# Kernel optimization log

Measured on AMD Instinct MI355X. Metric: run time of the kernel, lower is better.

Reference implementation:

```python
import jax, jax.numpy as jnp
import numpy as np

PLANE_SIZE = 512
N_LEVELS = 8
FEATURE_DIM = 16
N_PTS = 524288


def setup_inputs() -> dict:
    key = jax.random.key(0)
    k1, k2, k3 = jax.random.split(key, 3)
    x = jax.random.uniform(k1, (N_PTS, 3), dtype=jnp.float32)
    # per-point float mip level bias in [0, n_levels-1]
    level = jax.random.uniform(k2, (N_PTS, 1), dtype=jnp.float32) * (N_LEVELS - 1)
    fm = jax.random.uniform(k3, (3, PLANE_SIZE, PLANE_SIZE, FEATURE_DIM),
                            minval=-0.01, maxval=0.01, dtype=jnp.float32)
    return {"x": x, "level": level, "fm": fm, "n_levels": N_LEVELS}


def _bilinear(flat_pyr, offsets, sizes, uv, lvl_i):
    # flat_pyr: (3, T, C) concatenated mip levels; uv: (3, N, 2); lvl_i: (3, N) int32
    size = sizes[lvl_i]                      # (3, N) texture size at this mip
    fsize = size.astype(uv.dtype)
    px = uv[..., 0] * fsize - 0.5            # u -> width axis (nvdiffrast convention)
    py = uv[..., 1] * fsize - 0.5            # v -> height axis
    x0 = jnp.floor(px)
    y0 = jnp.floor(py)
    fx = (px - x0)[..., None]
    fy = (py - y0)[..., None]
    x0i = x0.astype(jnp.int32)
    y0i = y0.astype(jnp.int32)
    xa = jnp.clip(x0i, 0, size - 1)          # boundary_mode='clamp'
    xb = jnp.clip(x0i + 1, 0, size - 1)
    ya = jnp.clip(y0i, 0, size - 1)
    yb = jnp.clip(y0i + 1, 0, size - 1)
    base = offsets[lvl_i]
    p = jnp.arange(3)[:, None]
    g = lambda yy, xx: flat_pyr[p, base + yy * size + xx]   # (3, N, C) gather
    f00 = g(ya, xa); f01 = g(ya, xb); f10 = g(yb, xa); f11 = g(yb, xb)
    return (f00 * (1 - fx) + f01 * fx) * (1 - fy) + (f10 * (1 - fx) + f11 * fx) * fy


def reference(x, level, fm, n_levels):
    N = x.shape[0]
    C = fm.shape[-1]
    # build mip pyramid via 2x2 box filter (nvdiffrast auto-mips)
    levels = [fm]
    for _ in range(n_levels - 1):
        t = levels[-1]
        s = t.shape[1]
        levels.append(t.reshape(3, s // 2, 2, s // 2, 2, C).mean(axis=(2, 4)))
    sizes_list = [l.shape[1] for l in levels]
    offsets = jnp.asarray(np.cumsum([0] + [s * s for s in sizes_list[:-1]]), jnp.int32)
    sizes = jnp.asarray(sizes_list, jnp.int32)
    flat_pyr = jnp.concatenate([l.reshape(3, -1, C) for l in levels], axis=1)  # (3, T, C)
    # tri-plane decomposition: plane0 sees (y,z), plane1 (x,z), plane2 (x,y)
    uv = jnp.stack([x[:, [1, 2]], x[:, [0, 2]], x[:, [0, 1]]], axis=0)  # (3, N, 2)
    max_mip = n_levels - 1
    lvl = jnp.clip(jnp.broadcast_to(level.reshape(1, N), (3, N)), 0.0, float(max_mip))
    l0 = jnp.floor(lvl)
    f = (lvl - l0)[..., None]                # (3, N, 1) level fraction
    l0i = l0.astype(jnp.int32)
    l1i = jnp.minimum(l0i + 1, max_mip)
    s0 = _bilinear(flat_pyr, offsets, sizes, uv, l0i)
    s1 = _bilinear(flat_pyr, offsets, sizes, uv, l1i)
    enc = s0 * (1 - f) + s1 * f              # (3, N, C) trilinear (mip-lerped)
    # permute(1,2,0,3).view(N, 3C): per point, concat plane0|plane1|plane2 features
    return jnp.transpose(enc, (1, 0, 2)).reshape(N, 3 * C)
```

## Files before the change

### kernel.cpp

```cpp
#include <hip/hip_runtime.h>


#define FM_PLANE_STRIDE (262144 * 16)
#define WS_PLANE_STRIDE (87376 * 16)

__device__ __forceinline__ float4 ld4(const float* p) {
    return *reinterpret_cast<const float4*>(p);
}

__global__ __launch_bounds__(256) void mip_build(
    const float* __restrict__ src, float* __restrict__ dst,
    int ls, int srcPlaneStride, int dstPlaneStride)
{
    const int s = 1 << ls;
    int t = blockIdx.x * blockDim.x + threadIdx.x;
    const int perPlane = s * s * 4;
    if (t >= perPlane) return;
    const int p = blockIdx.y;
    const int q = t & 3;
    const int idx = t >> 2;
    const int y = idx >> ls;
    const int x = idx & (s - 1);
    const int ss = s << 1;
    const float* sp = src + (size_t)p * srcPlaneStride
                          + ((size_t)(2 * y) * ss + 2 * x) * 16 + q * 4;
    float4 a = ld4(sp);
    float4 b = ld4(sp + 16);
    float4 c = ld4(sp + (size_t)ss * 16);
    float4 d = ld4(sp + (size_t)ss * 16 + 16);
    float4 r;
    r.x = (a.x + b.x + c.x + d.x) * 0.25f;
    r.y = (a.y + b.y + c.y + d.y) * 0.25f;
    r.z = (a.z + b.z + c.z + d.z) * 0.25f;
    r.w = (a.w + b.w + c.w + d.w) * 0.25f;
    float* dp = dst + (size_t)p * dstPlaneStride + ((size_t)y * s + x) * 16 + q * 4;
    *reinterpret_cast<float4*>(dp) = r;
}

__device__ __forceinline__ float4 bilerp(
    const float* __restrict__ fm, const float* __restrict__ mips,
    int p, int l, float u, float v, int q)
{
    const int sz = 512 >> l;
    const float fsz = (float)sz;
    float px = u * fsz - 0.5f;
    float py = v * fsz - 0.5f;
    float xf = floorf(px);
    float yf = floorf(py);
    float fx = px - xf;
    float fy = py - yf;
    int xi = (int)xf;
    int yi = (int)yf;
    int xa = min(max(xi, 0), sz - 1);
    int xb = min(xi + 1, sz - 1);
    int ya = min(max(yi, 0), sz - 1);
    int yb = min(yi + 1, sz - 1);
    const float* base;
    if (l == 0) {
        base = fm + (size_t)p * FM_PLANE_STRIDE;
    } else {
        unsigned off = (262144u - ((unsigned)(sz * sz) << 2)) / 3u;
        base = mips + (size_t)p * WS_PLANE_STRIDE + (size_t)off * 16;
    }
    const float* r0 = base + (size_t)(ya * sz) * 16 + q * 4;
    const float* r1 = base + (size_t)(yb * sz) * 16 + q * 4;
    float4 f00 = ld4(r0 + xa * 16);
    float4 f01 = ld4(r0 + xb * 16);
    float4 f10 = ld4(r1 + xa * 16);
    float4 f11 = ld4(r1 + xb * 16);
    float gx = 1.f - fx, gy = 1.f - fy;
    float4 r;
    r.x = (f00.x * gx + f01.x * fx) * gy + (f10.x * gx + f11.x * fx) * fy;
    r.y = (f00.y * gx + f01.y * fx) * gy + (f10.y * gx + f11.y * fx) * fy;
    r.z = (f00.z * gx + f01.z * fx) * gy + (f10.z * gx + f11.z * fx) * fy;
    r.w = (f00.w * gx + f01.w * fx) * gy + (f10.w * gx + f11.w * fx) * fy;
    return r;
}

__global__ __launch_bounds__(256) void trimip_sample(
    const float* __restrict__ xyz, const float* __restrict__ level,
    const float* __restrict__ fm, const float* __restrict__ mips,
    float* __restrict__ out, int N)
{
    int t = blockIdx.x * blockDim.x + threadIdx.x;
    if (t >= N * 12) return;
    const int q = t & 3;
    const int r = t >> 2;
    const int n = r / 3;
    const int p = r - n * 3;

    const float c0 = xyz[n * 3 + 0];
    const float c1 = xyz[n * 3 + 1];
    const float c2 = xyz[n * 3 + 2];
    const float u = (p == 0) ? c1 : c0;
    const float v = (p == 2) ? c1 : c2;

    float lv = level[n];
    lv = fminf(fmaxf(lv, 0.f), 7.f);
    float lf = floorf(lv);
    float f = lv - lf;
    int l0 = (int)lf;
    int l1 = min(l0 + 1, 7);

    float4 s0 = bilerp(fm, mips, p, l0, u, v, q);
    float4 s1 = bilerp(fm, mips, p, l1, u, v, q);
    float g = 1.f - f;
    float4 o;
    o.x = s0.x * g + s1.x * f;
    o.y = s0.y * g + s1.y * f;
    o.z = s0.z * g + s1.z * f;
    o.w = s0.w * g + s1.w * f;
    reinterpret_cast<float4*>(out)[t] = o;
}

extern "C" void kernel_launch(void* const* d_in, const int* in_sizes, int n_in,
                              void* d_out, int out_size, void* d_ws, size_t ws_size,
                              hipStream_t stream) {
    const float* xyz   = (const float*)d_in[0];
    const float* level = (const float*)d_in[1];
    const float* fm    = (const float*)d_in[2];
    float* mips = (float*)d_ws;
    float* out  = (float*)d_out;
    const int N = in_sizes[1];

    unsigned off = 0;
    const float* src = fm;
    int srcStride = FM_PLANE_STRIDE;
    for (int l = 1; l <= 7; ++l) {
        const int s = 512 >> l;
        const int ls = 9 - l;
        float* dst = mips + (size_t)off * 16;
        const int perPlane = s * s * 4;
        dim3 grid((perPlane + 255) / 256, 3);
        mip_build<<<grid, dim3(256), 0, stream>>>(src, dst, ls, srcStride, WS_PLANE_STRIDE);
        src = dst;
        srcStride = WS_PLANE_STRIDE;
        off += s * s;
    }

    const int total = N * 12;
    const int blocks = (total + 255) / 256;
    trimip_sample<<<blocks, 256, 0, stream>>>(xyz, level, fm, mips, out, N);
}
```

Baseline: 219.3 us.

## Fuse mip levels 2-7 into one shared-memory tiled kernel

Replaces seven per-level mip_build launches with two: level 1 is built from the base texture, and one tiled kernel builds levels 2 through 7 from level 1. Each block holds a 32x32 tile in shared memory and reduces it down level by level. This removes five kernel launches and the global round trips between the small levels. The cost is fewer blocks in the tail kernel (192) and idle threads in its later stages.

```diff
diff --git a/kernel.cpp b/kernel.cpp
--- a/kernel.cpp
+++ b/kernel.cpp
@@ -7,34 +7,112 @@
 __device__ __forceinline__ float4 ld4(const float* p) {
     return *reinterpret_cast<const float4*>(p);
 }
+__device__ __forceinline__ void st4(float* p, float4 v) {
+    *reinterpret_cast<float4*>(p) = v;
+}
+__device__ __forceinline__ float4 avg4(float4 a, float4 b, float4 c, float4 d) {
+    float4 r;
+    r.x = (a.x + b.x + c.x + d.x) * 0.25f;
+    r.y = (a.y + b.y + c.y + d.y) * 0.25f;
+    r.z = (a.z + b.z + c.z + d.z) * 0.25f;
+    r.w = (a.w + b.w + c.w + d.w) * 0.25f;
+    return r;
+}
 
 __global__ __launch_bounds__(256) void mip_build(
-    const float* __restrict__ src, float* __restrict__ dst,
-    int ls, int srcPlaneStride, int dstPlaneStride)
-{
-    const int s = 1 << ls;
+    const float* __restrict__ src, float* __restrict__ dst)
+{
+    const int s = 256;
     int t = blockIdx.x * blockDim.x + threadIdx.x;
-    const int perPlane = s * s * 4;
-    if (t >= perPlane) return;
     const int p = blockIdx.y;
     const int q = t & 3;
     const int idx = t >> 2;
-    const int y = idx >> ls;
-    const int x = idx & (s - 1);
-    const int ss = s << 1;
-    const float* sp = src + (size_t)p * srcPlaneStride
+    const int y = idx >> 8;
+    const int x = idx & 255;
+    const int ss = 512;
+    const float* sp = src + (size_t)p * FM_PLANE_STRIDE
                           + ((size_t)(2 * y) * ss + 2 * x) * 16 + q * 4;
     float4 a = ld4(sp);
     float4 b = ld4(sp + 16);
     float4 c = ld4(sp + (size_t)ss * 16);
     float4 d = ld4(sp + (size_t)ss * 16 + 16);
-    float4 r;
-    r.x = (a.x + b.x + c.x + d.x) * 0.25f;
-    r.y = (a.y + b.y + c.y + d.y) * 0.25f;
-    r.z = (a.z + b.z + c.z + d.z) * 0.25f;
-    r.w = (a.w + b.w + c.w + d.w) * 0.25f;
-    float* dp = dst + (size_t)p * dstPlaneStride + ((size_t)y * s + x) * 16 + q * 4;
-    *reinterpret_cast<float4*>(dp) = r;
+    float* dp = dst + (size_t)p * WS_PLANE_STRIDE + ((size_t)y * s + x) * 16 + q * 4;
+    st4(dp, avg4(a, b, c, d));
+}
+
+__global__ __launch_bounds__(256) void mip_tail(float* __restrict__ mips)
+{
+    const int tile = blockIdx.x;
+    const int q    = blockIdx.y;
+    const int p    = blockIdx.z;
+    const int ty = tile >> 2, tx = tile & 3;
+    const int tid = threadIdx.x;
+
+    __shared__ float4 A[32 * 32];
+    __shared__ float4 B[16 * 16];
+
+    float* plane = mips + (size_t)p * WS_PLANE_STRIDE;
+    const float* L1 = plane;
+    float* L2 = plane + (size_t)65536 * 16;
+    float* L3 = plane + (size_t)81920 * 16;
+    float* L4 = plane + (size_t)86016 * 16;
+    float* L5 = plane + (size_t)87040 * 16;
+    float* L6 = plane + (size_t)87296 * 16;
+    float* L7 = plane + (size_t)87360 * 16;
+
+    #pragma unroll
+    for (int k = 0; k < 4; ++k) {
+        int li = tid + k * 256;
+        int ly = li >> 5, lx = li & 31;
+        int gy = ty * 32 + ly, gx = tx * 32 + lx;
+        const float* sp = L1 + ((size_t)(2 * gy) * 256 + 2 * gx) * 16 + q * 4;
+        float4 r = avg4(ld4(sp), ld4(sp + 16),
+                        ld4(sp + 256 * 16), ld4(sp + 256 * 16 + 16));
+        A[li] = r;
+        st4(L2 + ((size_t)gy * 128 + gx) * 16 + q * 4, r);
+    }
+    __syncthreads();
+
+    if (tid < 256) {
+        int ly = tid >> 4, lx = tid & 15;
+        float4 r = avg4(A[(2 * ly) * 32 + 2 * lx],     A[(2 * ly) * 32 + 2 * lx + 1],
+                        A[(2 * ly + 1) * 32 + 2 * lx], A[(2 * ly + 1) * 32 + 2 * lx + 1]);
+        B[tid] = r;
+        st4(L3 + ((size_t)(ty * 16 + ly) * 64 + tx * 16 + lx) * 16 + q * 4, r);
+    }
+    __syncthreads();
+
+    if (tid < 64) {
+        int ly = tid >> 3, lx = tid & 7;
+        float4 r = avg4(B[(2 * ly) * 16 + 2 * lx],     B[(2 * ly) * 16 + 2 * lx + 1],
+                        B[(2 * ly + 1) * 16 + 2 * lx], B[(2 * ly + 1) * 16 + 2 * lx + 1]);
+        A[tid] = r;
+        st4(L4 + ((size_t)(ty * 8 + ly) * 32 + tx * 8 + lx) * 16 + q * 4, r);
+    }
+    __syncthreads();
+
+    if (tid < 16) {
+        int ly = tid >> 2, lx = tid & 3;
+        float4 r = avg4(A[(2 * ly) * 8 + 2 * lx],     A[(2 * ly) * 8 + 2 * lx + 1],
+                        A[(2 * ly + 1) * 8 + 2 * lx], A[(2 * ly + 1) * 8 + 2 * lx + 1]);
+        B[tid] = r;
+        st4(L5 + ((size_t)(ty * 4 + ly) * 16 + tx * 4 + lx) * 16 + q * 4, r);
+    }
+    __syncthreads();
+
+    if (tid < 4) {
+        int ly = tid >> 1, lx = tid & 1;
+        float4 r = avg4(B[(2 * ly) * 4 + 2 * lx],     B[(2 * ly) * 4 + 2 * lx + 1],
+                        B[(2 * ly + 1) * 4 + 2 * lx], B[(2 * ly + 1) * 4 + 2 * lx + 1]);
+        A[tid] = r;
+        st4(L6 + ((size_t)(ty * 2 + ly) * 8 + tx * 2 + lx) * 16 + q * 4, r);
+    }
+    __syncthreads();
+
+    if (tid == 0) {
+        float4 r = avg4(A[0], A[1], A[2], A[3]);
+        st4(L7 + ((size_t)ty * 4 + tx) * 16 + q * 4, r);
+    }
 }
 
 __device__ __forceinline__ float4 bilerp(
@@ -123,20 +201,8 @@
     float* out  = (float*)d_out;
     const int N = in_sizes[1];
 
-    unsigned off = 0;
-    const float* src = fm;
-    int srcStride = FM_PLANE_STRIDE;
-    for (int l = 1; l <= 7; ++l) {
-        const int s = 512 >> l;
-        const int ls = 9 - l;
-        float* dst = mips + (size_t)off * 16;
-        const int perPlane = s * s * 4;
-        dim3 grid((perPlane + 255) / 256, 3);
-        mip_build<<<grid, dim3(256), 0, stream>>>(src, dst, ls, srcStride, WS_PLANE_STRIDE);
-        src = dst;
-        srcStride = WS_PLANE_STRIDE;
-        off += s * s;
-    }
+    mip_build<<<dim3(1024, 3), dim3(256), 0, stream>>>(fm, mips);
+    mip_tail<<<dim3(16, 4, 3), dim3(256), 0, stream>>>(mips);
 
     const int total = N * 12;
     const int blocks = (total + 255) / 256;
```

After: 211.2 us. 3.7% less time.
